# Kernel tuning notes

Hardware: AMD Instinct MI355X
Metric: run time of the kernel (lower is better)

The kernel has to match this reference:

```python
import jax, jax.numpy as jnp
import numpy as np

NB, B, C, L = 4, 16, 256, 4096
BN_EPS = 1e-5


def setup_inputs() -> dict:
    key = jax.random.key(0)
    ks = jax.random.split(key, 10)
    s = 0.02
    return {
        "x": jax.random.normal(ks[0], (NB, B, C, L), jnp.float32),
        "Wq": jax.random.normal(ks[1], (NB, C, C), jnp.float32) * s,
        "bq": jax.random.normal(ks[2], (NB, C), jnp.float32) * s,
        "Wk": jax.random.normal(ks[3], (NB, C, C), jnp.float32) * s,
        "bk": jax.random.normal(ks[4], (NB, C), jnp.float32) * s,
        "Wv": jax.random.normal(ks[5], (NB, C, C), jnp.float32) * s,
        "bv": jax.random.normal(ks[6], (NB, C), jnp.float32) * s,
        "Wo": jax.random.normal(ks[7], (NB, C, C), jnp.float32) * s,
        "bo": jax.random.normal(ks[8], (NB, C), jnp.float32) * s,
        "gamma": jnp.ones((NB, C), jnp.float32),
        "beta": jnp.zeros((NB, C), jnp.float32),
        "edge_w": jnp.ones((NB, NB), jnp.float32),
        "branch_imp": jnp.ones((NB,), jnp.float32),
    }


def _proj(W, b, x):
    # 1x1 Conv1d == per-branch channel mixing: [nb,o,c] x [nb,B,c,L] -> [nb,B,o,L]
    return jnp.einsum('noc,nbcl->nbol', W, x) + b[:, None, :, None]


def reference(x, Wq, bq, Wk, bk, Wv, bv, Wo, bo, gamma, beta, edge_w, branch_imp):
    feat_dim = x.shape[2]
    scale = jnp.sqrt(jnp.asarray(feat_dim, x.dtype))
    q = _proj(Wq, bq, x)
    k = _proj(Wk, bk, x)
    v = _proj(Wv, bv, x)
    # descriptors: [nb, B, C, 2] = (mean over L, max over L)
    qd = jnp.stack([q.mean(axis=-1), q.max(axis=-1)], axis=-1)
    kd = jnp.stack([k.mean(axis=-1), k.max(axis=-1)], axis=-1)
    # mean over 2x2 bmm entries == (sum_p qd)(sum_q kd) summed over C, / 4
    scores = jnp.einsum('ibcp,jbcq->ijb', qd, kd) / (4.0 * scale)
    scores = scores * edge_w[:, :, None]
    attn = jax.nn.softmax(scores, axis=1) * jax.nn.softmax(branch_imp)[None, :, None]
    # weighted aggregation over source branches j
    agg = jnp.einsum('ijb,jbcl->ibcl', attn, v)
    out = _proj(Wo, bo, agg)
    # BatchNorm1d (training-mode batch statistics over B and L per channel, per branch)
    mean = out.mean(axis=(1, 3), keepdims=True)
    var = out.var(axis=(1, 3), keepdims=True)
    bn = (out - mean) * jax.lax.rsqrt(var + BN_EPS)
    bn = bn * gamma[:, None, :, None] + beta[:, None, :, None]
    return jax.nn.relu(bn) + x
```

## Files before the change

kernel.cpp:

```cpp
#include <hip/hip_runtime.h>
#include <stdint.h>
#include <stddef.h>

#define NBR 4
#define BSZ 16
#define CHN 256
#define LEN 4096
#define NB_B 64
#define BL   65536
#define BN_EPS 1e-5f
#define W_EL (NBR*CHN*CHN)

typedef unsigned short ushortT;
typedef unsigned short ushort4_t __attribute__((ext_vector_type(4)));
typedef unsigned short ushort8_t __attribute__((ext_vector_type(8)));
typedef short bf16x8 __attribute__((ext_vector_type(8)));
typedef float f32x4 __attribute__((ext_vector_type(4)));

__device__ __forceinline__ float bf2f(ushortT u) {
    return __uint_as_float(((unsigned)u) << 16);
}
__device__ __forceinline__ ushortT f2bf(float f) {
    unsigned b = __float_as_uint(f);
    return (ushortT)((b + 0x7FFFu + ((b >> 16) & 1u)) >> 16);
}
__device__ __forceinline__ unsigned encf(float f) {
    unsigned b = __float_as_uint(f);
    return (b & 0x80000000u) ? ~b : (b | 0x80000000u);
}
__device__ __forceinline__ float decf(unsigned u) {
    unsigned b = (u & 0x80000000u) ? (u ^ 0x80000000u) : ~u;
    return __uint_as_float(b);
}

__device__ __forceinline__ int swzX(int row, int cb) {
    return row * 512 + (cb ^ ((row & 7) << 4) ^ (((row >> 3) & 3) << 7));
}

__device__ __forceinline__ void stage_x_f32(const float* x, ushortT* sX, int z, int lbase, int tid)
{
    const int ls = tid & 127;
    const int gh = tid >> 7;
    const float* xp = x + (size_t)z * CHN * LEN + lbase + ls;
#pragma unroll
    for (int g = 0; g < 16; ++g) {
        int c0 = (gh * 16 + g) * 8;
        ushort8_t u;
#pragma unroll
        for (int i = 0; i < 8; ++i) u[i] = f2bf(xp[(size_t)(c0 + i) * LEN]);
        *(ushort8_t*)((char*)sX + swzX(ls, c0 * 2)) = u;
    }
}
__device__ __forceinline__ void stage_x_bf16(const ushortT* a, ushortT* sX, int z, int lbase, int tid)
{
    const int ls = tid & 127;
    const int gh = tid >> 7;
    const ushortT* xp = a + (size_t)z * CHN * LEN + lbase + ls;
#pragma unroll
    for (int g = 0; g < 16; ++g) {
        int c0 = (gh * 16 + g) * 8;
        ushort8_t u;
#pragma unroll
        for (int i = 0; i < 8; ++i) u[i] = xp[(size_t)(c0 + i) * LEN];
        *(ushort8_t*)((char*)sX + swzX(ls, c0 * 2)) = u;
    }
}

__device__ __forceinline__ void mfma_chunk_frag(const ushortT* sX, const ushortT* __restrict__ Wb2,
                                                int otile, f32x4 acc[4][4],
                                                int wr, int wc, int lane, int kb)
{
    const int am = wr * 64 + (lane & 15);
    const int kg = (lane >> 4) * 16;
#pragma unroll
    for (int s = 0; s < 2; ++s) {
        const int cb = kb * 2 + s;
        bf16x8 a[4], b[4];
#pragma unroll
        for (int nf = 0; nf < 4; ++nf) {
            const int ob = otile * 8 + wc * 4 + nf;
            b[nf] = *(const bf16x8*)(Wb2 + (((size_t)ob * 8 + cb) * 64 + lane) * 8);
        }
#pragma unroll
        for (int mf = 0; mf < 4; ++mf)
            a[mf] = *(const bf16x8*)((const char*)sX + swzX(am + mf * 16, kb * 128 + s * 64 + kg));
#pragma unroll
        for (int mf = 0; mf < 4; ++mf)
#pragma unroll
            for (int nf = 0; nf < 4; ++nf)
                acc[mf][nf] = __builtin_amdgcn_mfma_f32_16x16x32_bf16(a[mf], b[nf], acc[mf][nf], 0, 0, 0);
    }
}

__global__ __launch_bounds__(256, 2)
void qkv_kernel(const float* __restrict__ x, const ushortT* __restrict__ Wbf,
                const float* __restrict__ bv,
                float* __restrict__ qsum, unsigned* __restrict__ qmax,
                float* __restrict__ ksum, unsigned* __restrict__ kmax,
                ushortT* __restrict__ vbuf)
{
    __shared__ ushortT sX[128 * 256];
    const int tid = threadIdx.x;
    const int lane = tid & 63;
    const int wv = tid >> 6;
    const int wr = wv >> 1, wc = wv & 1;
    const int lbase = blockIdx.x * 128;
    const int z = blockIdx.y;
    const int n = z >> 4;

    stage_x_f32(x, sX, z, lbase, tid);
    __syncthreads();

    const f32x4 z4 = {0.f, 0.f, 0.f, 0.f};

    for (int w = 0; w < 3; ++w) {
        const ushortT* Wb2 = Wbf + ((size_t)w * NBR + n) * CHN * CHN;
        for (int ot = 0; ot < 2; ++ot) {
            f32x4 acc[4][4];
#pragma unroll
            for (int mf = 0; mf < 4; ++mf)
#pragma unroll
                for (int nf = 0; nf < 4; ++nf) acc[mf][nf] = z4;
#pragma unroll
            for (int kb = 0; kb < 4; ++kb)
                mfma_chunk_frag(sX, Wb2, ot, acc, wr, wc, lane, kb);

            const int obase = ot * 128;
            if (w < 2) {
                float* rs = (w == 0) ? qsum : ksum;
                unsigned* rm = (w == 0) ? qmax : kmax;
#pragma unroll
                for (int nf = 0; nf < 4; ++nf) {
                    float s = 0.f, m = -3.4e38f;
#pragma unroll
                    for (int mf = 0; mf < 4; ++mf)
#pragma unroll
                        for (int r = 0; r < 4; ++r) {
                            float v = acc[mf][nf][r];
                            s += v; m = fmaxf(m, v);
                        }
                    s += __shfl_xor(s, 16); s += __shfl_xor(s, 32);
                    m = fmaxf(m, __shfl_xor(m, 16)); m = fmaxf(m, __shfl_xor(m, 32));
                    if (lane < 16) {
                        int o = obase + wc * 64 + nf * 16 + lane;
                        atomicAdd(&rs[z * CHN + o], s);
                        atomicMax(&rm[z * CHN + o], encf(m));
                    }
                }
            } else {
#pragma unroll
                for (int nf = 0; nf < 4; ++nf) {
                    int o = obase + wc * 64 + nf * 16 + (lane & 15);
                    float bvv = bv[n * CHN + o];
#pragma unroll
                    for (int mf = 0; mf < 4; ++mf) {
                        int l = lbase + wr * 64 + mf * 16 + ((lane >> 4) << 2);
                        ushort4_t u;
#pragma unroll
                        for (int r = 0; r < 4; ++r) u[r] = f2bf(acc[mf][nf][r] + bvv);
                        *(ushort4_t*)(vbuf + (size_t)(z * CHN + o) * LEN + l) = u;
                    }
                }
            }
        }
    }
}

__global__ __launch_bounds__(256, 2)
void ogemm_kernel(const ushortT* __restrict__ agg, const ushortT* __restrict__ Wbo,
                  const float* __restrict__ bo_,
                  float* __restrict__ bnsum, float* __restrict__ bnss,
                  ushortT* __restrict__ outpre)
{
    __shared__ ushortT sX[128 * 256];
    const int tid = threadIdx.x;
    const int lane = tid & 63;
    const int wv = tid >> 6;
    const int wr = wv >> 1, wc = wv & 1;
    const int lbase = blockIdx.x * 128;
    const int z = blockIdx.y;
    const int n = z >> 4;
    const ushortT* Wb2 = Wbo + (size_t)n * CHN * CHN;

    stage_x_bf16(agg, sX, z, lbase, tid);
    __syncthreads();

    const f32x4 z4 = {0.f, 0.f, 0.f, 0.f};
    for (int ot = 0; ot < 2; ++ot) {
        f32x4 acc[4][4];
#pragma unroll
        for (int mf = 0; mf < 4; ++mf)
#pragma unroll
            for (int nf = 0; nf < 4; ++nf) acc[mf][nf] = z4;
#pragma unroll
        for (int kb = 0; kb < 4; ++kb)
            mfma_chunk_frag(sX, Wb2, ot, acc, wr, wc, lane, kb);

        const int obase = ot * 128;
#pragma unroll
        for (int nf = 0; nf < 4; ++nf) {
            int o = obase + wc * 64 + nf * 16 + (lane & 15);
            float bb = bo_[n * CHN + o];
            float s = 0.f, q2 = 0.f;
#pragma unroll
            for (int mf = 0; mf < 4; ++mf) {
                int l = lbase + wr * 64 + mf * 16 + ((lane >> 4) << 2);
                ushort4_t u;
#pragma unroll
                for (int r = 0; r < 4; ++r) {
                    float v = acc[mf][nf][r] + bb;
                    u[r] = f2bf(v);
                    s += v; q2 += v * v;
                }
                *(ushort4_t*)(outpre + (size_t)(z * CHN + o) * LEN + l) = u;
            }
            s += __shfl_xor(s, 16); s += __shfl_xor(s, 32);
            q2 += __shfl_xor(q2, 16); q2 += __shfl_xor(q2, 32);
            if (lane < 16) {
                atomicAdd(&bnsum[n * CHN + o], s);
                atomicAdd(&bnss[n * CHN + o], q2);
            }
        }
    }
}

__global__ void wcvt_kernel(const float* __restrict__ Wq, const float* __restrict__ Wk,
                            const float* __restrict__ Wv, const float* __restrict__ Wo,
                            ushortT* __restrict__ Wbf)
{
    int t = blockIdx.x * 256 + threadIdx.x;
    if (t < 4 * (W_EL / 8)) {
        const float* srcs[4] = {Wq, Wk, Wv, Wo};
        int w    = t >> 15;
        int r    = t & 32767;
        int lane = r & 63;
        int cb   = (r >> 6) & 7;
        int ob   = (r >> 9) & 15;
        int n    = r >> 13;
        const float* src = srcs[w] + (size_t)n * CHN * CHN;
        int o = ob * 16 + (lane & 15);
        int c = cb * 32 + (lane >> 4) * 8;
        float4 f0 = *(const float4*)(src + (size_t)o * CHN + c);
        float4 f1 = *(const float4*)(src + (size_t)o * CHN + c + 4);
        ushort8_t u = {f2bf(f0.x), f2bf(f0.y), f2bf(f0.z), f2bf(f0.w),
                       f2bf(f1.x), f2bf(f1.y), f2bf(f1.z), f2bf(f1.w)};
        *(ushort8_t*)(Wbf + ((size_t)w * NBR + n) * CHN * CHN
                          + (((size_t)ob * 8 + cb) * 64 + lane) * 8) = u;
    }
}

__global__ void attn_kernel(const float* __restrict__ qsum, const unsigned* __restrict__ qmax,
                            const float* __restrict__ ksum, const unsigned* __restrict__ kmax,
                            const float* __restrict__ bq, const float* __restrict__ bk,
                            const float* __restrict__ edge, const float* __restrict__ bimp,
                            float* __restrict__ attn)
{
    __shared__ float sc[NBR][NBR][BSZ];
    int tid = threadIdx.x;
    int i = tid >> 6, j = (tid >> 4) & 3, b = tid & 15;
    float s = 0.f;
    const float invL = 1.0f / (float)LEN;
    for (int c = 0; c < CHN; ++c) {
        int qi = (i * BSZ + b) * CHN + c;
        int ki = (j * BSZ + b) * CHN + c;
        float sq = qsum[qi] * invL + decf(qmax[qi]) + 2.f * bq[i * CHN + c];
        float sk = ksum[ki] * invL + decf(kmax[ki]) + 2.f * bk[j * CHN + c];
        s += sq * sk;
    }
    sc[i][j][b] = s * edge[i * 4 + j] * (1.0f / 64.0f);
    __syncthreads();
    if (tid < 64) {
        int ii = tid >> 4, bb = tid & 15;
        float m = -3.4e38f;
        for (int jj = 0; jj < 4; ++jj) m = fmaxf(m, sc[ii][jj][bb]);
        float e[4]; float sum = 0.f;
        for (int jj = 0; jj < 4; ++jj) { e[jj] = __expf(sc[ii][jj][bb] - m); sum += e[jj]; }
        float bm = fmaxf(fmaxf(bimp[0], bimp[1]), fmaxf(bimp[2], bimp[3]));
        float be[4]; float bs = 0.f;
        for (int jj = 0; jj < 4; ++jj) { be[jj] = __expf(bimp[jj] - bm); bs += be[jj]; }
        for (int jj = 0; jj < 4; ++jj)
            attn[(ii * 4 + jj) * BSZ + bb] = (e[jj] / sum) * (be[jj] / bs);
    }
}

__global__ __launch_bounds__(256)
void agg_kernel(const ushortT* __restrict__ v, const float* __restrict__ attn,
                ushortT* __restrict__ agg)
{
    __shared__ float sa[256];
    sa[threadIdx.x] = attn[threadIdx.x];
    __syncthreads();
    const long long U = (long long)BSZ * CHN * (LEN / 8);
    for (long long u = (long long)blockIdx.x * blockDim.x + threadIdx.x; u < U;
         u += (long long)gridDim.x * blockDim.x) {
        int l0 = (int)(u & 511) * 8;
        int c  = (int)(u >> 9) & 255;
        int b  = (int)(u >> 17);
        float vv[4][8];
#pragma unroll
        for (int j = 0; j < 4; ++j) {
            ushort8_t raw = *(const ushort8_t*)(v + (((size_t)(j * BSZ + b) * CHN + c) * LEN) + l0);
#pragma unroll
            for (int e = 0; e < 8; ++e) vv[j][e] = bf2f(raw[e]);
        }
#pragma unroll
        for (int i = 0; i < 4; ++i) {
            float a0 = sa[(i * 4 + 0) * BSZ + b];
            float a1 = sa[(i * 4 + 1) * BSZ + b];
            float a2 = sa[(i * 4 + 2) * BSZ + b];
            float a3 = sa[(i * 4 + 3) * BSZ + b];
            ushort8_t out;
#pragma unroll
            for (int e = 0; e < 8; ++e) {
                float r = a0 * vv[0][e] + a1 * vv[1][e] + a2 * vv[2][e] + a3 * vv[3][e];
                out[e] = f2bf(r);
            }
            *(ushort8_t*)(agg + (((size_t)(i * BSZ + b) * CHN + c) * LEN) + l0) = out;
        }
    }
}

__global__ void bnfin_kernel(const float* __restrict__ bnsum, const float* __restrict__ bnss,
                             const float* __restrict__ gamma, const float* __restrict__ beta,
                             float* __restrict__ scl, float* __restrict__ shf)
{
    int t = blockIdx.x * blockDim.x + threadIdx.x;
    if (t < NBR * CHN) {
        const float inv = 1.0f / (float)BL;
        float mean = bnsum[t] * inv;
        float var = bnss[t] * inv - mean * mean;
        float rs = rsqrtf(var + BN_EPS);
        float s = gamma[t] * rs;
        scl[t] = s;
        shf[t] = beta[t] - mean * s;
    }
}

__global__ __launch_bounds__(256)
void final_kernel(const ushortT* __restrict__ outpre, const float* __restrict__ x,
                  const float* __restrict__ scl, const float* __restrict__ shf,
                  float* __restrict__ out)
{
    const long long U = (long long)NB_B * CHN * (LEN / 8);
    for (long long u = (long long)blockIdx.x * blockDim.x + threadIdx.x; u < U;
         u += (long long)gridDim.x * blockDim.x) {
        int l0 = (int)(u & 511) * 8;
        int c  = (int)(u >> 9) & 255;
        int zz = (int)(u >> 17);
        int n  = zz >> 4;
        size_t base = ((size_t)zz * CHN + c) * LEN + l0;
        ushort8_t op = *(const ushort8_t*)(outpre + base);
        float4 x0 = *(const float4*)(x + base);
        float4 x1 = *(const float4*)(x + base + 4);
        float sc = scl[n * CHN + c];
        float sh = shf[n * CHN + c];
        float xr[8] = {x0.x, x0.y, x0.z, x0.w, x1.x, x1.y, x1.z, x1.w};
        float res[8];
#pragma unroll
        for (int e = 0; e < 8; ++e) {
            float bn = bf2f(op[e]) * sc + sh;
            res[e] = fmaxf(bn, 0.f) + xr[e];
        }
        float4 o0 = {res[0], res[1], res[2], res[3]};
        float4 o1 = {res[4], res[5], res[6], res[7]};
        *(float4*)(out + base) = o0;
        *(float4*)(out + base + 4) = o1;
    }
}

extern "C" void kernel_launch(void* const* d_in, const int* in_sizes, int n_in,
                              void* d_out, int out_size, void* d_ws, size_t ws_size,
                              hipStream_t stream)
{
    const float* x     = (const float*)d_in[0];
    const float* Wq    = (const float*)d_in[1];
    const float* bq    = (const float*)d_in[2];
    const float* Wk    = (const float*)d_in[3];
    const float* bk    = (const float*)d_in[4];
    const float* Wv    = (const float*)d_in[5];
    const float* bv    = (const float*)d_in[6];
    const float* Wo    = (const float*)d_in[7];
    const float* bo    = (const float*)d_in[8];
    const float* gamma = (const float*)d_in[9];
    const float* beta  = (const float*)d_in[10];
    const float* edge  = (const float*)d_in[11];
    const float* bimp  = (const float*)d_in[12];

    char* ws = (char*)d_ws;
    const size_t V_BYTES = (size_t)NBR * BSZ * CHN * LEN * 2;
    ushortT* vbuf = (ushortT*)ws;
    size_t off = V_BYTES;
    float*    qsum = (float*)(ws + off);    off += 65536;
    unsigned* qmax = (unsigned*)(ws + off); off += 65536;
    float*    ksum = (float*)(ws + off);    off += 65536;
    unsigned* kmax = (unsigned*)(ws + off); off += 65536;
    float*    attn = (float*)(ws + off);    off += 1024;
    float*    bnsum= (float*)(ws + off);    off += 4096;
    float*    bnss = (float*)(ws + off);    off += 4096;
    float*    scl  = (float*)(ws + off);    off += 4096;
    float*    shf  = (float*)(ws + off);    off += 4096;

    hipMemsetAsync(ws + V_BYTES, 0, off - V_BYTES, stream);

    ushortT* aggbuf = (ushortT*)d_out;
    ushortT* Wbf = (ushortT*)((char*)d_out + ((size_t)134217728));
    float*   outf = (float*)d_out;

    wcvt_kernel<<<(4 * (W_EL / 8) + 255) / 256, 256, 0, stream>>>(Wq, Wk, Wv, Wo, Wbf);

    dim3 gq(LEN / 128, NB_B);
    qkv_kernel<<<gq, 256, 0, stream>>>(x, Wbf, bv, qsum, qmax, ksum, kmax, vbuf);
    attn_kernel<<<1, 256, 0, stream>>>(qsum, qmax, ksum, kmax, bq, bk, edge, bimp, attn);
    agg_kernel<<<2048, 256, 0, stream>>>(vbuf, attn, aggbuf);
    ogemm_kernel<<<gq, 256, 0, stream>>>(aggbuf, Wbf + (size_t)3 * W_EL, bo, bnsum, bnss, vbuf);
    bnfin_kernel<<<4, 256, 0, stream>>>(bnsum, bnss, gamma, beta, scl, shf);
    final_kernel<<<8192, 256, 0, stream>>>(vbuf, x, scl, shf, outf);
}
```

Baseline: 521.6 us.

## Fuse attention aggregation into output GEMM staging and shrink L tile to 64

Removes the separate aggregation kernel. The output projection GEMM now builds its shared-memory input directly as an attention-weighted sum of the four branch V tensors, so the bf16 agg buffer no longer has to be written and read back through HBM. The L tile is also halved from 128 to 64, and each wave now computes a 64x32 output slice, with launch bounds raised so more blocks can be resident per CU. The cost is that each output-GEMM block reads four V slices, and V is reread once per output branch, so the V read traffic from the old agg kernel moves into the GEMM staging path. Buffers are reshuffled so V lives in the output memory and the pre-BN output lives in the workspace.

```diff
diff --git a/kernel.cpp b/kernel.cpp
--- a/kernel.cpp
+++ b/kernel.cpp
@@ -10,6 +10,7 @@
 #define BL   65536
 #define BN_EPS 1e-5f
 #define W_EL (NBR*CHN*CHN)
+#define LT   64
 
 typedef unsigned short ushortT;
 typedef unsigned short ushort4_t __attribute__((ext_vector_type(4)));
@@ -39,46 +40,56 @@
 
 __device__ __forceinline__ void stage_x_f32(const float* x, ushortT* sX, int z, int lbase, int tid)
 {
-    const int ls = tid & 127;
-    const int gh = tid >> 7;
+    const int ls = tid & 63;
+    const int gh = tid >> 6;
     const float* xp = x + (size_t)z * CHN * LEN + lbase + ls;
 #pragma unroll
-    for (int g = 0; g < 16; ++g) {
-        int c0 = (gh * 16 + g) * 8;
+    for (int g = 0; g < 8; ++g) {
+        int c0 = (gh * 8 + g) * 8;
         ushort8_t u;
 #pragma unroll
         for (int i = 0; i < 8; ++i) u[i] = f2bf(xp[(size_t)(c0 + i) * LEN]);
         *(ushort8_t*)((char*)sX + swzX(ls, c0 * 2)) = u;
     }
 }
-__device__ __forceinline__ void stage_x_bf16(const ushortT* a, ushortT* sX, int z, int lbase, int tid)
-{
-    const int ls = tid & 127;
-    const int gh = tid >> 7;
-    const ushortT* xp = a + (size_t)z * CHN * LEN + lbase + ls;
-#pragma unroll
-    for (int g = 0; g < 16; ++g) {
-        int c0 = (gh * 16 + g) * 8;
+
+__device__ __forceinline__ void stage_agg(const ushortT* v, ushortT* sX, const float aj[4],
+                                          int b_, int lbase, int tid)
+{
+    const int ls = tid & 63;
+    const int gh = tid >> 6;
+    const ushortT* vp0 = v + (size_t)(0 * BSZ + b_) * CHN * LEN + lbase + ls;
+    const ushortT* vp1 = v + (size_t)(1 * BSZ + b_) * CHN * LEN + lbase + ls;
+    const ushortT* vp2 = v + (size_t)(2 * BSZ + b_) * CHN * LEN + lbase + ls;
+    const ushortT* vp3 = v + (size_t)(3 * BSZ + b_) * CHN * LEN + lbase + ls;
+#pragma unroll
+    for (int g = 0; g < 8; ++g) {
+        int c0 = (gh * 8 + g) * 8;
         ushort8_t u;
 #pragma unroll
-        for (int i = 0; i < 8; ++i) u[i] = xp[(size_t)(c0 + i) * LEN];
+        for (int i = 0; i < 8; ++i) {
+            size_t o = (size_t)(c0 + i) * LEN;
+            float s = aj[0] * bf2f(vp0[o]) + aj[1] * bf2f(vp1[o])
+                    + aj[2] * bf2f(vp2[o]) + aj[3] * bf2f(vp3[o]);
+            u[i] = f2bf(s);
+        }
         *(ushort8_t*)((char*)sX + swzX(ls, c0 * 2)) = u;
     }
 }
 
 __device__ __forceinline__ void mfma_chunk_frag(const ushortT* sX, const ushortT* __restrict__ Wb2,
-                                                int otile, f32x4 acc[4][4],
-                                                int wr, int wc, int lane, int kb)
-{
-    const int am = wr * 64 + (lane & 15);
+                                                int otile, f32x4 acc[4][2],
+                                                int wc, int lane, int kb)
+{
+    const int am = lane & 15;
     const int kg = (lane >> 4) * 16;
 #pragma unroll
     for (int s = 0; s < 2; ++s) {
         const int cb = kb * 2 + s;
-        bf16x8 a[4], b[4];
-#pragma unroll
-        for (int nf = 0; nf < 4; ++nf) {
-            const int ob = otile * 8 + wc * 4 + nf;
+        bf16x8 a[4], b[2];
+#pragma unroll
+        for (int nf = 0; nf < 2; ++nf) {
+            const int ob = otile * 8 + wc * 2 + nf;
             b[nf] = *(const bf16x8*)(Wb2 + (((size_t)ob * 8 + cb) * 64 + lane) * 8);
         }
 #pragma unroll
@@ -87,24 +98,23 @@
 #pragma unroll
         for (int mf = 0; mf < 4; ++mf)
 #pragma unroll
-            for (int nf = 0; nf < 4; ++nf)
+            for (int nf = 0; nf < 2; ++nf)
                 acc[mf][nf] = __builtin_amdgcn_mfma_f32_16x16x32_bf16(a[mf], b[nf], acc[mf][nf], 0, 0, 0);
     }
 }
 
-__global__ __launch_bounds__(256, 2)
+__global__ __launch_bounds__(256, 5)
 void qkv_kernel(const float* __restrict__ x, const ushortT* __restrict__ Wbf,
                 const float* __restrict__ bv,
                 float* __restrict__ qsum, unsigned* __restrict__ qmax,
                 float* __restrict__ ksum, unsigned* __restrict__ kmax,
                 ushortT* __restrict__ vbuf)
 {
-    __shared__ ushortT sX[128 * 256];
+    __shared__ ushortT sX[LT * 256];
     const int tid = threadIdx.x;
     const int lane = tid & 63;
-    const int wv = tid >> 6;
-    const int wr = wv >> 1, wc = wv & 1;
-    const int lbase = blockIdx.x * 128;
+    const int wc = tid >> 6;
+    const int lbase = blockIdx.x * LT;
     const int z = blockIdx.y;
     const int n = z >> 4;
 
@@ -116,21 +126,21 @@
     for (int w = 0; w < 3; ++w) {
         const ushortT* Wb2 = Wbf + ((size_t)w * NBR + n) * CHN * CHN;
         for (int ot = 0; ot < 2; ++ot) {
-            f32x4 acc[4][4];
+            f32x4 acc[4][2];
 #pragma unroll
             for (int mf = 0; mf < 4; ++mf)
 #pragma unroll
-                for (int nf = 0; nf < 4; ++nf) acc[mf][nf] = z4;
+                for (int nf = 0; nf < 2; ++nf) acc[mf][nf] = z4;
 #pragma unroll
             for (int kb = 0; kb < 4; ++kb)
-                mfma_chunk_frag(sX, Wb2, ot, acc, wr, wc, lane, kb);
-
-            const int obase = ot * 128;
+                mfma_chunk_frag(sX, Wb2, ot, acc, wc, lane, kb);
+
+            const int obase = ot * 128 + wc * 32;
             if (w < 2) {
                 float* rs = (w == 0) ? qsum : ksum;
                 unsigned* rm = (w == 0) ? qmax : kmax;
 #pragma unroll
-                for (int nf = 0; nf < 4; ++nf) {
+                for (int nf = 0; nf < 2; ++nf) {
                     float s = 0.f, m = -3.4e38f;
 #pragma unroll
                     for (int mf = 0; mf < 4; ++mf)
@@ -142,19 +152,19 @@
                     s += __shfl_xor(s, 16); s += __shfl_xor(s, 32);
                     m = fmaxf(m, __shfl_xor(m, 16)); m = fmaxf(m, __shfl_xor(m, 32));
                     if (lane < 16) {
-                        int o = obase + wc * 64 + nf * 16 + lane;
+                        int o = obase + nf * 16 + lane;
                         atomicAdd(&rs[z * CHN + o], s);
                         atomicMax(&rm[z * CHN + o], encf(m));
                     }
                 }
             } else {
 #pragma unroll
-                for (int nf = 0; nf < 4; ++nf) {
-                    int o = obase + wc * 64 + nf * 16 + (lane & 15);
+                for (int nf = 0; nf < 2; ++nf) {
+                    int o = obase + nf * 16 + (lane & 15);
                     float bvv = bv[n * CHN + o];
 #pragma unroll
                     for (int mf = 0; mf < 4; ++mf) {
-                        int l = lbase + wr * 64 + mf * 16 + ((lane >> 4) << 2);
+                        int l = lbase + mf * 16 + ((lane >> 4) << 2);
                         ushort4_t u;
 #pragma unroll
                         for (int r = 0; r < 4; ++r) u[r] = f2bf(acc[mf][nf][r] + bvv);
@@ -166,51 +176,55 @@
     }
 }
 
-__global__ __launch_bounds__(256, 2)
-void ogemm_kernel(const ushortT* __restrict__ agg, const ushortT* __restrict__ Wbo,
-                  const float* __restrict__ bo_,
+__global__ __launch_bounds__(256, 5)
+void ogemm_kernel(const ushortT* __restrict__ v, const ushortT* __restrict__ Wbo,
+                  const float* __restrict__ attn, const float* __restrict__ bo_,
                   float* __restrict__ bnsum, float* __restrict__ bnss,
                   ushortT* __restrict__ outpre)
 {
-    __shared__ ushortT sX[128 * 256];
+    __shared__ ushortT sX[LT * 256];
     const int tid = threadIdx.x;
     const int lane = tid & 63;
-    const int wv = tid >> 6;
-    const int wr = wv >> 1, wc = wv & 1;
-    const int lbase = blockIdx.x * 128;
+    const int wc = tid >> 6;
+    const int lbase = blockIdx.x * LT;
     const int z = blockIdx.y;
     const int n = z >> 4;
+    const int b_ = z & 15;
     const ushortT* Wb2 = Wbo + (size_t)n * CHN * CHN;
 
-    stage_x_bf16(agg, sX, z, lbase, tid);
+    float aj[4];
+#pragma unroll
+    for (int j = 0; j < 4; ++j) aj[j] = attn[(n * 4 + j) * BSZ + b_];
+
+    stage_agg(v, sX, aj, b_, lbase, tid);
     __syncthreads();
 
     const f32x4 z4 = {0.f, 0.f, 0.f, 0.f};
     for (int ot = 0; ot < 2; ++ot) {
-        f32x4 acc[4][4];
+        f32x4 acc[4][2];
 #pragma unroll
         for (int mf = 0; mf < 4; ++mf)
 #pragma unroll
-            for (int nf = 0; nf < 4; ++nf) acc[mf][nf] = z4;
+            for (int nf = 0; nf < 2; ++nf) acc[mf][nf] = z4;
 #pragma unroll
         for (int kb = 0; kb < 4; ++kb)
-            mfma_chunk_frag(sX, Wb2, ot, acc, wr, wc, lane, kb);
-
-        const int obase = ot * 128;
-#pragma unroll
-        for (int nf = 0; nf < 4; ++nf) {
-            int o = obase + wc * 64 + nf * 16 + (lane & 15);
+            mfma_chunk_frag(sX, Wb2, ot, acc, wc, lane, kb);
+
+        const int obase = ot * 128 + wc * 32;
+#pragma unroll
+        for (int nf = 0; nf < 2; ++nf) {
+            int o = obase + nf * 16 + (lane & 15);
             float bb = bo_[n * CHN + o];
             float s = 0.f, q2 = 0.f;
 #pragma unroll
             for (int mf = 0; mf < 4; ++mf) {
-                int l = lbase + wr * 64 + mf * 16 + ((lane >> 4) << 2);
+                int l = lbase + mf * 16 + ((lane >> 4) << 2);
                 ushort4_t u;
 #pragma unroll
                 for (int r = 0; r < 4; ++r) {
-                    float v = acc[mf][nf][r] + bb;
-                    u[r] = f2bf(v);
-                    s += v; q2 += v * v;
+                    float vv = acc[mf][nf][r] + bb;
+                    u[r] = f2bf(vv);
+                    s += vv; q2 += vv * vv;
                 }
                 *(ushort4_t*)(outpre + (size_t)(z * CHN + o) * LEN + l) = u;
             }
@@ -283,43 +297,6 @@
     }
 }
 
-__global__ __launch_bounds__(256)
-void agg_kernel(const ushortT* __restrict__ v, const float* __restrict__ attn,
-                ushortT* __restrict__ agg)
-{
-    __shared__ float sa[256];
-    sa[threadIdx.x] = attn[threadIdx.x];
-    __syncthreads();
-    const long long U = (long long)BSZ * CHN * (LEN / 8);
-    for (long long u = (long long)blockIdx.x * blockDim.x + threadIdx.x; u < U;
-         u += (long long)gridDim.x * blockDim.x) {
-        int l0 = (int)(u & 511) * 8;
-        int c  = (int)(u >> 9) & 255;
-        int b  = (int)(u >> 17);
-        float vv[4][8];
-#pragma unroll
-        for (int j = 0; j < 4; ++j) {
-            ushort8_t raw = *(const ushort8_t*)(v + (((size_t)(j * BSZ + b) * CHN + c) * LEN) + l0);
-#pragma unroll
-            for (int e = 0; e < 8; ++e) vv[j][e] = bf2f(raw[e]);
-        }
-#pragma unroll
-        for (int i = 0; i < 4; ++i) {
-            float a0 = sa[(i * 4 + 0) * BSZ + b];
-            float a1 = sa[(i * 4 + 1) * BSZ + b];
-            float a2 = sa[(i * 4 + 2) * BSZ + b];
-            float a3 = sa[(i * 4 + 3) * BSZ + b];
-            ushort8_t out;
-#pragma unroll
-            for (int e = 0; e < 8; ++e) {
-                float r = a0 * vv[0][e] + a1 * vv[1][e] + a2 * vv[2][e] + a3 * vv[3][e];
-                out[e] = f2bf(r);
-            }
-            *(ushort8_t*)(agg + (((size_t)(i * BSZ + b) * CHN + c) * LEN) + l0) = out;
-        }
-    }
-}
-
 __global__ void bnfin_kernel(const float* __restrict__ bnsum, const float* __restrict__ bnss,
                              const float* __restrict__ gamma, const float* __restrict__ beta,
                              float* __restrict__ scl, float* __restrict__ shf)
@@ -387,9 +364,9 @@
     const float* bimp  = (const float*)d_in[12];
 
     char* ws = (char*)d_ws;
-    const size_t V_BYTES = (size_t)NBR * BSZ * CHN * LEN * 2;
-    ushortT* vbuf = (ushortT*)ws;
-    size_t off = V_BYTES;
+    const size_t P_BYTES = (size_t)NBR * BSZ * CHN * LEN * 2;
+    ushortT* outpre = (ushortT*)ws;
+    size_t off = P_BYTES;
     float*    qsum = (float*)(ws + off);    off += 65536;
     unsigned* qmax = (unsigned*)(ws + off); off += 65536;
     float*    ksum = (float*)(ws + off);    off += 65536;
@@ -400,19 +377,18 @@
     float*    scl  = (float*)(ws + off);    off += 4096;
     float*    shf  = (float*)(ws + off);    off += 4096;
 
-    hipMemsetAsync(ws + V_BYTES, 0, off - V_BYTES, stream);
-
-    ushortT* aggbuf = (ushortT*)d_out;
-    ushortT* Wbf = (ushortT*)((char*)d_out + ((size_t)134217728));
+    hipMemsetAsync(ws + P_BYTES, 0, off - P_BYTES, stream);
+
+    ushortT* vbuf = (ushortT*)d_out;
+    ushortT* Wbf  = (ushortT*)((char*)d_out + ((size_t)134217728));
     float*   outf = (float*)d_out;
 
     wcvt_kernel<<<(4 * (W_EL / 8) + 255) / 256, 256, 0, stream>>>(Wq, Wk, Wv, Wo, Wbf);
 
-    dim3 gq(LEN / 128, NB_B);
+    dim3 gq(LEN / LT, NB_B);
     qkv_kernel<<<gq, 256, 0, stream>>>(x, Wbf, bv, qsum, qmax, ksum, kmax, vbuf);
     attn_kernel<<<1, 256, 0, stream>>>(qsum, qmax, ksum, kmax, bq, bk, edge, bimp, attn);
-    agg_kernel<<<2048, 256, 0, stream>>>(vbuf, attn, aggbuf);
-    ogemm_kernel<<<gq, 256, 0, stream>>>(aggbuf, Wbf + (size_t)3 * W_EL, bo, bnsum, bnss, vbuf);
+    ogemm_kernel<<<gq, 256, 0, stream>>>(vbuf, Wbf + (size_t)3 * W_EL, attn, bo, bnsum, bnss, outpre);
     bnfin_kernel<<<4, 256, 0, stream>>>(bnsum, bnss, gamma, beta, scl, shf);
-    final_kernel<<<8192, 256, 0, stream>>>(vbuf, x, scl, shf, outf);
-}
+    final_kernel<<<8192, 256, 0, stream>>>(outpre, x, scl, shf, outf);
+}
```

After: 883.1 us. 69.3% more time.
